# Performance work log

Measured on AMD Instinct MI355X. Metric: run time of the kernel, lower is better.

Reference implementation:

```python
import jax, jax.numpy as jnp
import numpy as np

D_MODEL = 1024
NUM_HEADS = 16
D_K = D_MODEL // NUM_HEADS
D_FF = 4096
EPS = 1e-5


def setup_inputs() -> dict:
    key = jax.random.key(0)
    ks = jax.random.split(key, 16)
    B, S = 2, 2048
    s_attn = 1.0 / np.sqrt(D_MODEL)
    s_ff1 = 1.0 / np.sqrt(D_MODEL)
    s_ff2 = 1.0 / np.sqrt(D_FF)
    return {
        "x": jax.random.normal(ks[0], (B, S, D_MODEL), jnp.float32),
        "Wq": jax.random.normal(ks[1], (D_MODEL, D_MODEL), jnp.float32) * s_attn,
        "bq": jnp.zeros((D_MODEL,), jnp.float32),
        "Wk": jax.random.normal(ks[2], (D_MODEL, D_MODEL), jnp.float32) * s_attn,
        "bk": jnp.zeros((D_MODEL,), jnp.float32),
        "Wv": jax.random.normal(ks[3], (D_MODEL, D_MODEL), jnp.float32) * s_attn,
        "bv": jnp.zeros((D_MODEL,), jnp.float32),
        "Wo": jax.random.normal(ks[4], (D_MODEL, D_MODEL), jnp.float32) * s_attn,
        "bo": jnp.zeros((D_MODEL,), jnp.float32),
        "W1": jax.random.normal(ks[5], (D_MODEL, D_FF), jnp.float32) * s_ff1,
        "b1": jnp.zeros((D_FF,), jnp.float32),
        "W2": jax.random.normal(ks[6], (D_FF, D_MODEL), jnp.float32) * s_ff2,
        "b2": jnp.zeros((D_MODEL,), jnp.float32),
        "g1": jnp.ones((D_MODEL,), jnp.float32),
        "be1": jnp.zeros((D_MODEL,), jnp.float32),
        "g2": jnp.ones((D_MODEL,), jnp.float32),
        "be2": jnp.zeros((D_MODEL,), jnp.float32),
    }


def _layernorm(x, g, b):
    m = jnp.mean(x, axis=-1, keepdims=True)
    v = jnp.mean(jnp.square(x - m), axis=-1, keepdims=True)
    return (x - m) * jax.lax.rsqrt(v + EPS) * g + b


def _split_heads(x, B, S):
    # (B, S, D) -> (B, H, S, d_k)
    return x.reshape(B, S, NUM_HEADS, D_K).transpose(0, 2, 1, 3)


def reference(x, Wq, bq, Wk, bk, Wv, bv, Wo, bo, W1, b1, W2, b2, g1, be1, g2, be2):
    B, S, _ = x.shape
    Q = _split_heads(x @ Wq + bq, B, S)
    K = _split_heads(x @ Wk + bk, B, S)
    V = _split_heads(x @ Wv + bv, B, S)
    scores = jnp.einsum("bhqd,bhkd->bhqk", Q, K) / np.sqrt(D_K).astype(np.float32)
    attn = jax.nn.softmax(scores, axis=-1)  # dropout is identity (p=0 / eval)
    ctx = jnp.einsum("bhqk,bhkd->bhqd", attn, V)
    ctx = ctx.transpose(0, 2, 1, 3).reshape(B, S, D_MODEL)
    attn_out = ctx @ Wo + bo
    h = _layernorm(x + attn_out, g1, be1)
    ff = jax.nn.relu(h @ W1 + b1) @ W2 + b2
    out = _layernorm(h + ff, g2, be2)
    return out, attn
```

## Files before the change

### kernel.cpp

```cpp
#include <hip/hip_runtime.h>
#include <cstddef>
#include <cstdint>

#define D_MODEL 1024
#define NUM_HEADS 16
#define DK 64
#define D_FF 4096
#define SEQ 2048
#define BATCH 2
#define EPS 1e-5f

typedef unsigned short u16;
typedef __attribute__((ext_vector_type(8))) short bf16x8;
typedef __attribute__((ext_vector_type(8))) unsigned short us8;
typedef __attribute__((ext_vector_type(4))) unsigned short us4;
typedef __attribute__((ext_vector_type(4))) float f32x4;

#define SBAR() asm volatile("s_barrier" ::: "memory")

__device__ __forceinline__ u16 f2b(float f) {
    unsigned u = __float_as_uint(f);
    u += 0x7fffu + ((u >> 16) & 1u);
    return (u16)(u >> 16);
}
__device__ __forceinline__ float b2f(u16 v) {
    return __uint_as_float((unsigned)v << 16);
}

__device__ __forceinline__ void gload16(const void* g, void* l) {
    __builtin_amdgcn_global_load_lds(
        (const __attribute__((address_space(1))) void*)g,
        (__attribute__((address_space(3))) void*)l, 16, 0, 0);
}

__device__ __forceinline__ void stage_half(
    const u16* __restrict__ g, int ld, long kbase, int h,
    u16* dst, int tid, int wid)
{
#pragma unroll
    for (int r = 0; r < 2; ++r) {
        const int ci  = r * 512 + tid;
        const int row = ci >> 2;
        const int wd  = ci & 3;
        const int f   = (row + (row >> 2)) & 3;
        const long src = (long)row * ld + kbase + (long)(h * 4 + (wd ^ f)) * 8;
        gload16(g + src, dst + (r * 512 + wid * 64) * 8);
    }
}

__device__ __forceinline__ bf16x8 frag64(const u16* base, int ks, int row, int g) {
    const int f = (row + (row >> 2)) & 3;
    return *(const bf16x8*)&base[ks * 8192 + row * 32 + ((g ^ f) * 8)];
}

template<int KTOT, bool RELU>
__global__ __launch_bounds__(512, 2) void gemm256(
    const u16* __restrict__ Abf, const u16* __restrict__ BT,
    const float* __restrict__ bias0, u16* __restrict__ C0,
    int ldc, int nx)
{
    constexpr int NT = KTOT / 64;
    __shared__ u16 lds[2][32768];

    const int tid = threadIdx.x;
    const int wid = tid >> 6, l = tid & 63;
    const int r16 = l & 15, g = l >> 4;
    const int wr = wid >> 2, wc = wid & 3;

    const int nwg = gridDim.x;
    const int q = nwg >> 3, rr = nwg & 7;
    const int xcd = blockIdx.x & 7, idx = blockIdx.x >> 3;
    const int wg = (xcd < rr ? xcd * (q + 1) : rr * (q + 1) + (xcd - rr) * q) + idx;
    const long bm = (long)(wg / nx) * 256;
    const long bn = (long)(wg % nx) * 256;

    const u16* Ag = Abf + bm * KTOT;
    const u16* Bg = BT + bn * KTOT;

    f32x4 acc[8][4];
#pragma unroll
    for (int i = 0; i < 8; ++i)
#pragma unroll
        for (int n = 0; n < 4; ++n)
            acc[i][n] = (f32x4){0.f, 0.f, 0.f, 0.f};

    stage_half(Ag, KTOT, 0, 0, &lds[0][0],     tid, wid);
    stage_half(Ag, KTOT, 0, 1, &lds[0][8192],  tid, wid);
    stage_half(Bg, KTOT, 0, 0, &lds[0][16384], tid, wid);
    stage_half(Bg, KTOT, 0, 1, &lds[0][24576], tid, wid);
    if (NT > 1) {
        stage_half(Ag, KTOT, 64, 0, &lds[1][0],     tid, wid);
        stage_half(Bg, KTOT, 64, 0, &lds[1][16384], tid, wid);
    }
    asm volatile("s_waitcnt vmcnt(4)" ::: "memory");
    SBAR();

    for (int t = 0; t < NT; ++t) {
        u16* cur = &lds[t & 1][0];
        u16* nxt = &lds[(t + 1) & 1][0];
        const long k1 = (long)(t + 1) * 64;
        const long k2 = (long)(t + 2) * 64;
        const bool s1 = (t + 1 < NT), s2 = (t + 2 < NT);

        bf16x8 a0[4], b0[4];
#pragma unroll
        for (int i = 0; i < 4; ++i) {
            a0[i] = frag64(cur,         0, wr * 128 + i * 16 + r16, g);
            b0[i] = frag64(cur + 16384, 0, wc * 64  + i * 16 + r16, g);
        }
        if (s1) stage_half(Ag, KTOT, k1, 1, nxt + 8192, tid, wid);
        SBAR();
        __builtin_amdgcn_s_setprio(1);
#pragma unroll
        for (int i = 0; i < 4; ++i)
#pragma unroll
            for (int n = 0; n < 4; ++n)
                acc[i][n] = __builtin_amdgcn_mfma_f32_16x16x32_bf16(
                    a0[i], b0[n], acc[i][n], 0, 0, 0);
        __builtin_amdgcn_s_setprio(0);
        SBAR();

        bf16x8 a1[4];
#pragma unroll
        for (int i = 0; i < 4; ++i)
            a1[i] = frag64(cur, 0, wr * 128 + (i + 4) * 16 + r16, g);
        if (s1) stage_half(Bg, KTOT, k1, 1, nxt + 24576, tid, wid);
        SBAR();
        __builtin_amdgcn_s_setprio(1);
#pragma unroll
        for (int i = 0; i < 4; ++i)
#pragma unroll
            for (int n = 0; n < 4; ++n)
                acc[i + 4][n] = __builtin_amdgcn_mfma_f32_16x16x32_bf16(
                    a1[i], b0[n], acc[i + 4][n], 0, 0, 0);
        __builtin_amdgcn_s_setprio(0);
        SBAR();

        bf16x8 a2[4], b1[4];
#pragma unroll
        for (int i = 0; i < 4; ++i) {
            a2[i] = frag64(cur,         1, wr * 128 + i * 16 + r16, g);
            b1[i] = frag64(cur + 16384, 1, wc * 64  + i * 16 + r16, g);
        }
        if (s2) stage_half(Ag, KTOT, k2, 0, cur, tid, wid);
        SBAR();
        __builtin_amdgcn_s_setprio(1);
#pragma unroll
        for (int i = 0; i < 4; ++i)
#pragma unroll
            for (int n = 0; n < 4; ++n)
                acc[i][n] = __builtin_amdgcn_mfma_f32_16x16x32_bf16(
                    a2[i], b1[n], acc[i][n], 0, 0, 0);
        __builtin_amdgcn_s_setprio(0);
        SBAR();

        bf16x8 a3[4];
#pragma unroll
        for (int i = 0; i < 4; ++i)
            a3[i] = frag64(cur, 1, wr * 128 + (i + 4) * 16 + r16, g);
        if (s2) stage_half(Bg, KTOT, k2, 0, cur + 16384, tid, wid);
        SBAR();
        __builtin_amdgcn_s_setprio(1);
#pragma unroll
        for (int i = 0; i < 4; ++i)
#pragma unroll
            for (int n = 0; n < 4; ++n)
                acc[i + 4][n] = __builtin_amdgcn_mfma_f32_16x16x32_bf16(
                    a3[i], b1[n], acc[i + 4][n], 0, 0, 0);
        __builtin_amdgcn_s_setprio(0);
        if (s2)      asm volatile("s_waitcnt vmcnt(4)" ::: "memory");
        else if (s1) asm volatile("s_waitcnt vmcnt(0)" ::: "memory");
        SBAR();
    }

    const long crow0 = bm + wr * 128 + g * 4;
    const long ccol0 = bn + wc * 64 + r16;
#pragma unroll
    for (int n = 0; n < 4; ++n) {
        const long col = ccol0 + n * 16;
        const float bv = bias0[col];
#pragma unroll
        for (int i = 0; i < 8; ++i)
#pragma unroll
            for (int j = 0; j < 4; ++j) {
                const long row = crow0 + i * 16 + j;
                float v = acc[i][n][j] + bv;
                if (RELU) v = fmaxf(v, 0.f);
                C0[row * (long)ldc + col] = f2b(v);
            }
    }
}

template<bool RELU, int NSPLIT>
__global__ __launch_bounds__(256) void gemm_mfma(
    const u16* __restrict__ Abf, const u16* __restrict__ BT,
    const float* __restrict__ bias0, const float* __restrict__ bias1,
    const float* __restrict__ bias2,
    u16* __restrict__ C0, u16* __restrict__ C1, u16* __restrict__ C2,
    int lda, int ldb, int ldc, int K, int nx)
{
    constexpr int BM = 128, BN = 128;
    constexpr int MI = 4, NI = 4;
    constexpr int RA = 2, RB = 2;
    constexpr int TILE = (BM + BN) * 32;

    __shared__ u16 sm[2][TILE];

    const int tid = threadIdx.x;
    const int w = tid >> 6, l = tid & 63;
    const int r16 = l & 15, g = l >> 4;
    const int wr = w >> 1, wc = w & 1;

    const int nwg = gridDim.x;
    const int q = nwg >> 3, rr = nwg & 7;
    const int xcd = blockIdx.x & 7, idx = blockIdx.x >> 3;
    const int wg = (xcd < rr ? xcd * (q + 1) : rr * (q + 1) + (xcd - rr) * q) + idx;
    const long bm = (long)(wg / nx) * BM;
    const long bn = (long)(wg % nx) * BN;

    f32x4 acc[MI][NI];
#pragma unroll
    for (int mi = 0; mi < MI; ++mi)
#pragma unroll
        for (int ni = 0; ni < NI; ++ni)
            acc[mi][ni] = (f32x4){0.f, 0.f, 0.f, 0.f};

    long aOff[RA], bOff[RB];
#pragma unroll
    for (int r = 0; r < RA; ++r) {
        int c = r * 256 + tid;
        aOff[r] = (long)(bm + (c >> 2)) * lda + (c & 3) * 8;
    }
#pragma unroll
    for (int r = 0; r < RB; ++r) {
        int c = r * 256 + tid;
        bOff[r] = (long)(bn + (c >> 2)) * ldb + (c & 3) * 8;
    }

#pragma unroll
    for (int r = 0; r < RA; ++r)
        gload16(Abf + aOff[r], &sm[0][0] + (r * 256 + w * 64) * 8);
#pragma unroll
    for (int r = 0; r < RB; ++r)
        gload16(BT + bOff[r], &sm[0][BM * 32] + (r * 256 + w * 64) * 8);
    __syncthreads();

    int cur = 0;
    for (int k0 = 0; k0 < K; k0 += 32) {
        if (k0 + 32 < K) {
            const int nxt = cur ^ 1;
#pragma unroll
            for (int r = 0; r < RA; ++r)
                gload16(Abf + aOff[r] + k0 + 32, &sm[nxt][0] + (r * 256 + w * 64) * 8);
#pragma unroll
            for (int r = 0; r < RB; ++r)
                gload16(BT + bOff[r] + k0 + 32, &sm[nxt][BM * 32] + (r * 256 + w * 64) * 8);
        }

        const u16* smA = &sm[cur][0];
        const u16* smB = &sm[cur][BM * 32];
        bf16x8 af[MI], bfr[NI];
#pragma unroll
        for (int mi = 0; mi < MI; ++mi)
            af[mi] = *(const bf16x8*)&smA[(wr * 64 + mi * 16 + r16) * 32 + g * 8];
#pragma unroll
        for (int ni = 0; ni < NI; ++ni)
            bfr[ni] = *(const bf16x8*)&smB[(wc * 64 + ni * 16 + r16) * 32 + g * 8];
#pragma unroll
        for (int mi = 0; mi < MI; ++mi)
#pragma unroll
            for (int ni = 0; ni < NI; ++ni)
                acc[mi][ni] = __builtin_amdgcn_mfma_f32_16x16x32_bf16(
                    af[mi], bfr[ni], acc[mi][ni], 0, 0, 0);

        __syncthreads();
        cur ^= 1;
    }

    const long crow0 = bm + wr * 64 + g * 4;

    if (NSPLIT == 3 && bn >= 2048) {
        const int btok = (int)(crow0 >> 11);
        const int kr0  = (int)(crow0 & 2047);
        const long ccolV = bn + wc * 64 + r16 - 2048;
#pragma unroll
        for (int ni = 0; ni < NI; ++ni) {
            const long col = ccolV + ni * 16;
            const int h = (int)(col >> 6), d = (int)(col & 63);
            const float bv = bias2[col];
            const long vrow = ((long)(btok * 16 + h) * 64 + d) * (long)SEQ;
#pragma unroll
            for (int mi = 0; mi < MI; ++mi) {
                us4 pv;
#pragma unroll
                for (int j = 0; j < 4; ++j)
                    pv[j] = f2b(acc[mi][ni][j] + bv);
                *(us4*)&C2[vrow + kr0 + mi * 16] = pv;
            }
        }
        return;
    }

    u16* Cb = C0; const float* bp = bias0; long coff = 0;
    if (NSPLIT == 3) {
        const int grp = (int)(bn >> 10);
        if (grp == 1) { Cb = C1; bp = bias1; }
        coff = (long)grp << 10;
    }
    const long ccol0 = bn + wc * 64 + r16 - coff;
#pragma unroll
    for (int ni = 0; ni < NI; ++ni) {
        const long col = ccol0 + ni * 16;
        const float bv = bp[col];
#pragma unroll
        for (int mi = 0; mi < MI; ++mi) {
#pragma unroll
            for (int j = 0; j < 4; ++j) {
                const long row = crow0 + mi * 16 + j;
                float v = acc[mi][ni][j] + bv;
                if (RELU) v = fmaxf(v, 0.f);
                Cb[row * (long)ldc + col] = f2b(v);
            }
        }
    }
}

#define QBLK 128
#define KBLK 64
#define NTT (SEQ / KBLK)
#define C2E 0.18033688f

__global__ __launch_bounds__(256) void flash_attn(
    const u16* __restrict__ Qg, const u16* __restrict__ Kg,
    const u16* __restrict__ Vt, float* __restrict__ attn,
    u16* __restrict__ ctx)
{
    __shared__ u16 smem[16384];
    __shared__ u16 Ps[4][2048];

    u16* const Qs  = smem;
    u16* const kb0 = smem + 8192;
    u16* const kb1 = smem;

    const int tid = threadIdx.x;
    const int w = tid >> 6, l = tid & 63;
    const int r16 = l & 15, g = l >> 4;

    const int wg = (blockIdx.x & 7) * (gridDim.x >> 3) + (blockIdx.x >> 3);
    const int qb = wg & 15, z = wg >> 4;
    const int b = z >> 4, h = z & 15;
    const long q0 = (long)qb * QBLK;

    const long kBase = ((long)b * SEQ) * D_MODEL + h * DK;
    const long vBase = (long)z * DK * SEQ;

#pragma unroll
    for (int r = 0; r < 4; ++r) {
        int c = r * 256 + tid;
        int row = c >> 3, bl = c & 7;
        long src = ((long)b * SEQ + q0 + row) * D_MODEL + h * DK
                 + ((bl ^ (row & 7)) * 8);
        gload16(Qg + src, Qs + (r * 256 + w * 64) * 8);
    }
#pragma unroll
    for (int r = 0; r < 2; ++r) {
        int c = r * 256 + tid;
        int row = c >> 3, bl = c & 7;
        gload16(Kg + kBase + (long)row * D_MODEL + ((bl ^ (row & 7)) * 8),
                kb0 + (r * 256 + w * 64) * 8);
    }
    __syncthreads();

    bf16x8 qf[2][2];
#pragma unroll
    for (int qi = 0; qi < 2; ++qi)
#pragma unroll
        for (int ks = 0; ks < 2; ++ks)
            qf[qi][ks] = *(const bf16x8*)
                &Qs[(w * 32 + qi * 16 + r16) * 64 + (((ks * 4 + g) ^ (r16 & 7)) * 8)];
    __syncthreads();

    float lrun[2] = {0.f, 0.f};

    for (int t = 0; t < NTT; ++t) {
        if (t + 1 < NTT) {
            u16* kdst = ((t + 1) & 1) ? kb1 : kb0;
            const long kro = (long)(t + 1) * KBLK;
#pragma unroll
            for (int r = 0; r < 2; ++r) {
                int c = r * 256 + tid;
                int row = c >> 3, bl = c & 7;
                gload16(Kg + kBase + (kro + row) * D_MODEL + ((bl ^ (row & 7)) * 8),
                        kdst + (r * 256 + w * 64) * 8);
            }
        }
        const u16* kcur = (t & 1) ? kb1 : kb0;

        f32x4 sT[4][2];
#pragma unroll
        for (int ki = 0; ki < 4; ++ki)
#pragma unroll
            for (int qi = 0; qi < 2; ++qi) sT[ki][qi] = (f32x4){0.f, 0.f, 0.f, 0.f};

        __builtin_amdgcn_s_setprio(1);
#pragma unroll
        for (int ks = 0; ks < 2; ++ks) {
            bf16x8 kf[4];
#pragma unroll
            for (int ki = 0; ki < 4; ++ki)
                kf[ki] = *(const bf16x8*)
                    &kcur[(ki * 16 + r16) * 64 + (((ks * 4 + g) ^ (r16 & 7)) * 8)];
#pragma unroll
            for (int ki = 0; ki < 4; ++ki)
#pragma unroll
                for (int qi = 0; qi < 2; ++qi)
                    sT[ki][qi] = __builtin_amdgcn_mfma_f32_16x16x32_bf16(
                        kf[ki], qf[qi][ks], sT[ki][qi], 0, 0, 0);
        }
        __builtin_amdgcn_s_setprio(0);

#pragma unroll
        for (int qi = 0; qi < 2; ++qi) {
            float ls = 0.f;
#pragma unroll
            for (int ki = 0; ki < 4; ++ki)
#pragma unroll
                for (int j = 0; j < 4; ++j)
                    ls += exp2f(sT[ki][qi][j] * C2E);
            ls += __shfl_xor(ls, 16);
            ls += __shfl_xor(ls, 32);
            lrun[qi] += ls;
        }
        __syncthreads();
    }

    const float il[2] = {1.0f / lrun[0], 1.0f / lrun[1]};

    u16* const p2b0 = smem + 8192;
    u16* const p2b1 = smem;
#pragma unroll
    for (int r = 0; r < 2; ++r) {
        int c = r * 256 + tid;
        int row = c >> 3, bl = c & 7;
        gload16(Kg + kBase + (long)row * D_MODEL + ((bl ^ (row & 7)) * 8),
                p2b0 + (r * 256 + w * 64) * 8);
        gload16(Vt + vBase + (long)row * SEQ + ((bl ^ (row & 7)) * 8),
                p2b0 + 4096 + (r * 256 + w * 64) * 8);
    }
    __syncthreads();

    f32x4 acc2[2][4];
#pragma unroll
    for (int mi = 0; mi < 2; ++mi)
#pragma unroll
        for (int ni = 0; ni < 4; ++ni) acc2[mi][ni] = (f32x4){0.f, 0.f, 0.f, 0.f};

    const long arow0 = ((long)z * SEQ + q0 + w * 32) * (long)SEQ;

    for (int t = 0; t < NTT; ++t) {
        const int k0 = t * KBLK;
        if (t + 1 < NTT) {
            u16* dst = ((t + 1) & 1) ? p2b1 : p2b0;
            const long kro = (long)(t + 1) * KBLK;
#pragma unroll
            for (int r = 0; r < 2; ++r) {
                int c = r * 256 + tid;
                int row = c >> 3, bl = c & 7;
                gload16(Kg + kBase + (kro + row) * D_MODEL + ((bl ^ (row & 7)) * 8),
                        dst + (r * 256 + w * 64) * 8);
                gload16(Vt + vBase + (long)row * SEQ + kro + ((bl ^ (row & 7)) * 8),
                        dst + 4096 + (r * 256 + w * 64) * 8);
            }
        }
        const u16* kcur = (t & 1) ? p2b1 : p2b0;
        const u16* vcur = kcur + 4096;

        f32x4 sT[4][2];
#pragma unroll
        for (int ki = 0; ki < 4; ++ki)
#pragma unroll
            for (int qi = 0; qi < 2; ++qi) sT[ki][qi] = (f32x4){0.f, 0.f, 0.f, 0.f};

        __builtin_amdgcn_s_setprio(1);
#pragma unroll
        for (int ks = 0; ks < 2; ++ks) {
            bf16x8 kf[4];
#pragma unroll
            for (int ki = 0; ki < 4; ++ki)
                kf[ki] = *(const bf16x8*)
                    &kcur[(ki * 16 + r16) * 64 + (((ks * 4 + g) ^ (r16 & 7)) * 8)];
#pragma unroll
            for (int ki = 0; ki < 4; ++ki)
#pragma unroll
                for (int qi = 0; qi < 2; ++qi)
                    sT[ki][qi] = __builtin_amdgcn_mfma_f32_16x16x32_bf16(
                        kf[ki], qf[qi][ks], sT[ki][qi], 0, 0, 0);
        }
        __builtin_amdgcn_s_setprio(0);

#pragma unroll
        for (int qi = 0; qi < 2; ++qi) {
            const long ar = arow0 + (long)(qi * 16 + r16) * SEQ + k0 + g * 4;
            const int prow = (qi * 16 + r16) * 64;
#pragma unroll
            for (int ki = 0; ki < 4; ++ki) {
                f32x4 p;
                p[0] = exp2f(sT[ki][qi][0] * C2E) * il[qi];
                p[1] = exp2f(sT[ki][qi][1] * C2E) * il[qi];
                p[2] = exp2f(sT[ki][qi][2] * C2E) * il[qi];
                p[3] = exp2f(sT[ki][qi][3] * C2E) * il[qi];
                __builtin_nontemporal_store(p, (f32x4*)&attn[ar + ki * 16]);
                us4 pb;
                pb[0] = f2b(p[0]); pb[1] = f2b(p[1]);
                pb[2] = f2b(p[2]); pb[3] = f2b(p[3]);
                const int kblk = 2 * ki + (g >> 1);
                *(us4*)&Ps[w][prow + ((kblk ^ (r16 & 7)) << 3) + ((g & 1) << 2)] = pb;
            }
        }

        __builtin_amdgcn_s_setprio(1);
#pragma unroll
        for (int ks = 0; ks < 2; ++ks) {
            bf16x8 pf[2], vf[4];
#pragma unroll
            for (int mi = 0; mi < 2; ++mi)
                pf[mi] = *(const bf16x8*)
                    &Ps[w][(mi * 16 + r16) * 64 + (((ks * 4 + g) ^ (r16 & 7)) << 3)];
#pragma unroll
            for (int ni = 0; ni < 4; ++ni)
                vf[ni] = *(const bf16x8*)
                    &vcur[(ni * 16 + r16) * 64 + (((ks * 4 + g) ^ (r16 & 7)) * 8)];
#pragma unroll
            for (int mi = 0; mi < 2; ++mi)
#pragma unroll
                for (int ni = 0; ni < 4; ++ni)
                    acc2[mi][ni] = __builtin_amdgcn_mfma_f32_16x16x32_bf16(
                        pf[mi], vf[ni], acc2[mi][ni], 0, 0, 0);
        }
        __builtin_amdgcn_s_setprio(0);
        __syncthreads();
    }

#pragma unroll
    for (int mi = 0; mi < 2; ++mi)
#pragma unroll
        for (int j = 0; j < 4; ++j) {
            const long grow = (long)b * SEQ + q0 + w * 32 + mi * 16 + g * 4 + j;
#pragma unroll
            for (int ni = 0; ni < 4; ++ni)
                ctx[grow * D_MODEL + h * DK + ni * 16 + r16] = f2b(acc2[mi][ni][j]);
        }
}

__device__ __forceinline__ void tr32(
    const float* __restrict__ W, u16* __restrict__ Wt, int R, int C,
    int bx, int by, int tx, int ty, float (*t)[33])
{
    const long c = (long)bx * 32 + tx;
    const long r0 = (long)by * 32;
#pragma unroll
    for (int j = 0; j < 32; j += 8)
        t[ty + j][tx] = W[(r0 + ty + j) * C + c];
    __syncthreads();
    const long r = r0 + tx;
#pragma unroll
    for (int j = 0; j < 32; j += 8)
        Wt[((long)bx * 32 + ty + j) * R + r] = f2b(t[tx][ty + j]);
}

__global__ __launch_bounds__(256) void preproc(
    const float* __restrict__ x, u16* __restrict__ x_bf,
    const float* __restrict__ Wq, const float* __restrict__ Wk,
    const float* __restrict__ Wv, const float* __restrict__ Wo,
    u16* __restrict__ Wqkvo_t,
    const float* __restrict__ W1, u16* __restrict__ W1t,
    const float* __restrict__ W2, u16* __restrict__ W2t)
{
    __shared__ float t[32][33];
    int bid = blockIdx.x;
    const int tx = threadIdx.x & 31, ty = threadIdx.x >> 5;

    if (bid < 2048) {
        long i = ((long)bid * 256 + threadIdx.x) * 8;
        float4 a = *(const float4*)(x + i);
        float4 b = *(const float4*)(x + i + 4);
        us8 o;
        o[0] = f2b(a.x); o[1] = f2b(a.y); o[2] = f2b(a.z); o[3] = f2b(a.w);
        o[4] = f2b(b.x); o[5] = f2b(b.y); o[6] = f2b(b.z); o[7] = f2b(b.w);
        *(us8*)(x_bf + i) = o;
        return;
    }
    bid -= 2048;
    if (bid < 4096) {
        const int z = bid >> 10, rem = bid & 1023;
        const float* W = (z == 0) ? Wq : (z == 1) ? Wk : (z == 2) ? Wv : Wo;
        tr32(W, Wqkvo_t + (size_t)z * D_MODEL * D_MODEL, D_MODEL, D_MODEL,
             rem & 31, rem >> 5, tx, ty, t);
        return;
    }
    bid -= 4096;
    if (bid < 4096) {
        tr32(W1, W1t, D_MODEL, D_FF, bid & 127, bid >> 7, tx, ty, t);
        return;
    }
    bid -= 4096;
    {
        tr32(W2, W2t, D_FF, D_MODEL, bid & 31, bid >> 5, tx, ty, t);
    }
}

template<int OM>
__global__ __launch_bounds__(256) void add_ln_kernel(
    const u16* __restrict__ a, const u16* __restrict__ b,
    const float* __restrict__ g, const float* __restrict__ be,
    void* __restrict__ outp)
{
    const int l = threadIdx.x & 63, w = threadIdx.x >> 6;
    const long row = (long)blockIdx.x * 4 + w;
    const long base = row * D_MODEL;

    float xv[16];
#pragma unroll
    for (int c = 0; c < 2; ++c) {
        const long off = c * 512 + l * 8;
        us8 av = *(const us8*)(a + base + off);
        us8 bv = *(const us8*)(b + base + off);
#pragma unroll
        for (int i = 0; i < 8; ++i)
            xv[c * 8 + i] = b2f(av[i]) + b2f(bv[i]);
    }

    float s = 0.f;
#pragma unroll
    for (int i = 0; i < 16; ++i) s += xv[i];
#pragma unroll
    for (int off = 1; off < 64; off <<= 1) s += __shfl_xor(s, off);
    const float mean = s * (1.0f / D_MODEL);

    float ss = 0.f;
#pragma unroll
    for (int i = 0; i < 16; ++i) {
        xv[i] -= mean;
        ss += xv[i] * xv[i];
    }
#pragma unroll
    for (int off = 1; off < 64; off <<= 1) ss += __shfl_xor(ss, off);
    const float rs = rsqrtf(ss * (1.0f / D_MODEL) + EPS);

#pragma unroll
    for (int c = 0; c < 2; ++c) {
        const long off = c * 512 + l * 8;
        float4 g0 = *(const float4*)(g + off);
        float4 g1 = *(const float4*)(g + off + 4);
        float4 b0 = *(const float4*)(be + off);
        float4 b1 = *(const float4*)(be + off + 4);
        float o[8];
        o[0] = xv[c*8+0] * rs * g0.x + b0.x;
        o[1] = xv[c*8+1] * rs * g0.y + b0.y;
        o[2] = xv[c*8+2] * rs * g0.z + b0.z;
        o[3] = xv[c*8+3] * rs * g0.w + b0.w;
        o[4] = xv[c*8+4] * rs * g1.x + b1.x;
        o[5] = xv[c*8+5] * rs * g1.y + b1.y;
        o[6] = xv[c*8+6] * rs * g1.z + b1.z;
        o[7] = xv[c*8+7] * rs * g1.w + b1.w;
        if (OM == 0) {
            float4 v0 = {o[0], o[1], o[2], o[3]};
            float4 v1 = {o[4], o[5], o[6], o[7]};
            *(float4*)((float*)outp + base + off) = v0;
            *(float4*)((float*)outp + base + off + 4) = v1;
        } else {
            us8 ob;
#pragma unroll
            for (int i = 0; i < 8; ++i) ob[i] = f2b(o[i]);
            *(us8*)((u16*)outp + base + off) = ob;
        }
    }
}

extern "C" void kernel_launch(void* const* d_in, const int* in_sizes, int n_in,
                              void* d_out, int out_size, void* d_ws, size_t ws_size,
                              hipStream_t stream)
{
    const float* x   = (const float*)d_in[0];
    const float* Wq  = (const float*)d_in[1];
    const float* bq  = (const float*)d_in[2];
    const float* Wk  = (const float*)d_in[3];
    const float* bk  = (const float*)d_in[4];
    const float* Wv  = (const float*)d_in[5];
    const float* bv  = (const float*)d_in[6];
    const float* Wo  = (const float*)d_in[7];
    const float* bo  = (const float*)d_in[8];
    const float* W1  = (const float*)d_in[9];
    const float* b1  = (const float*)d_in[10];
    const float* W2  = (const float*)d_in[11];
    const float* b2  = (const float*)d_in[12];
    const float* g1  = (const float*)d_in[13];
    const float* be1 = (const float*)d_in[14];
    const float* g2  = (const float*)d_in[15];
    const float* be2 = (const float*)d_in[16];

    float* out  = (float*)d_out;
    float* attn = out + (size_t)BATCH * SEQ * D_MODEL;

    char* ws = (char*)d_ws;
    const size_t MB = 1u << 20;
    u16* x_bf    = (u16*)(ws);
    u16* Q_bf    = (u16*)(ws + 8 * MB);
    u16* K_bf    = (u16*)(ws + 16 * MB);
    u16* Vt      = (u16*)(ws + 24 * MB);
    u16* spare   = (u16*)(ws + 32 * MB);
    u16* Wqkvo_t = (u16*)(ws + 40 * MB);
    u16* W1t     = (u16*)(ws + 48 * MB);
    u16* W2t     = (u16*)(ws + 56 * MB);
    u16* ff1_bf  = (u16*)(ws + 64 * MB);
    u16* ctx_bf  = (u16*)(ws + 96 * MB);
    u16* Wot     = Wqkvo_t + (size_t)3 * D_MODEL * D_MODEL;
    u16* h_bf    = K_bf;
    u16* ao_bf   = spare;
    u16* ff2_bf  = Vt;

    const int M = BATCH * SEQ;
    dim3 T(256);

    preproc<<<dim3(2048 + 3 * 4096), T, 0, stream>>>(
        x, x_bf, Wq, Wk, Wv, Wo, Wqkvo_t, W1, W1t, W2, W2t);

    gemm_mfma<false, 3><<<dim3((M / 128) * 24), T, 0, stream>>>(
        x_bf, Wqkvo_t, bq, bk, bv, Q_bf, K_bf, Vt,
        D_MODEL, D_MODEL, D_MODEL, D_MODEL, 24);

    flash_attn<<<dim3((SEQ / QBLK) * BATCH * NUM_HEADS), T, 0, stream>>>(
        Q_bf, K_bf, Vt, attn, ctx_bf);

    gemm_mfma<false, 1><<<dim3((M / 128) * 8), T, 0, stream>>>(
        ctx_bf, Wot, bo, nullptr, nullptr, ao_bf, nullptr, nullptr,
        D_MODEL, D_MODEL, D_MODEL, D_MODEL, 8);

    add_ln_kernel<1><<<dim3(M / 4), T, 0, stream>>>(x_bf, ao_bf, g1, be1, h_bf);

    gemm256<D_MODEL, true><<<dim3((M / 256) * (D_FF / 256)), dim3(512), 0, stream>>>(
        h_bf, W1t, b1, ff1_bf, D_FF, D_FF / 256);

    gemm_mfma<false, 1><<<dim3((M / 128) * 8), T, 0, stream>>>(
        ff1_bf, W2t, b2, nullptr, nullptr, ff2_bf, nullptr, nullptr,
        D_FF, D_FF, D_MODEL, D_FF, 8);

    add_ln_kernel<0><<<dim3(M / 4), T, 0, stream>>>(h_bf, ff2_bf, g2, be2, out);
}
```

Before: 424.8 us.

## Add 128x64 GEMM for N=1024 projections and split V transpose into separate kernel

Adds a new gemm_n64 kernel with 128x64 tiles and uses it for the Wo and W2 projections. This doubles the number of workgroups on the N=1024 GEMMs (512 instead of 256) to fill more compute units, at the cost of more A-tile reloads. The fused transposed V store in the QKV GEMM epilogue is replaced by a plain row-major store plus a separate shared-memory transpose kernel. That removes the strided scatter writes but adds an extra launch and an extra pass over V.

```diff
diff --git a/kernel.cpp b/kernel.cpp
--- a/kernel.cpp
+++ b/kernel.cpp
@@ -277,36 +277,14 @@
         cur ^= 1;
     }
 
-    const long crow0 = bm + wr * 64 + g * 4;
-
-    if (NSPLIT == 3 && bn >= 2048) {
-        const int btok = (int)(crow0 >> 11);
-        const int kr0  = (int)(crow0 & 2047);
-        const long ccolV = bn + wc * 64 + r16 - 2048;
-#pragma unroll
-        for (int ni = 0; ni < NI; ++ni) {
-            const long col = ccolV + ni * 16;
-            const int h = (int)(col >> 6), d = (int)(col & 63);
-            const float bv = bias2[col];
-            const long vrow = ((long)(btok * 16 + h) * 64 + d) * (long)SEQ;
-#pragma unroll
-            for (int mi = 0; mi < MI; ++mi) {
-                us4 pv;
-#pragma unroll
-                for (int j = 0; j < 4; ++j)
-                    pv[j] = f2b(acc[mi][ni][j] + bv);
-                *(us4*)&C2[vrow + kr0 + mi * 16] = pv;
-            }
-        }
-        return;
-    }
-
     u16* Cb = C0; const float* bp = bias0; long coff = 0;
     if (NSPLIT == 3) {
         const int grp = (int)(bn >> 10);
-        if (grp == 1) { Cb = C1; bp = bias1; }
+        if (grp == 1)      { Cb = C1; bp = bias1; }
+        else if (grp == 2) { Cb = C2; bp = bias2; }
         coff = (long)grp << 10;
     }
+    const long crow0 = bm + wr * 64 + g * 4;
     const long ccol0 = bn + wc * 64 + r16 - coff;
 #pragma unroll
     for (int ni = 0; ni < NI; ++ni) {
@@ -320,6 +298,108 @@
                 float v = acc[mi][ni][j] + bv;
                 if (RELU) v = fmaxf(v, 0.f);
                 Cb[row * (long)ldc + col] = f2b(v);
+            }
+        }
+    }
+}
+
+template<bool RELU>
+__global__ __launch_bounds__(256) void gemm_n64(
+    const u16* __restrict__ Abf, const u16* __restrict__ BT,
+    const float* __restrict__ bias, u16* __restrict__ C,
+    int lda, int ldb, int ldc, int K, int nx)
+{
+    constexpr int BM = 128, BN = 64;
+    constexpr int MI = 2, NI = 4;
+    constexpr int RA = 2, RB = 1;
+    constexpr int TILE = (BM + BN) * 32;
+
+    __shared__ u16 sm[2][TILE];
+
+    const int tid = threadIdx.x;
+    const int w = tid >> 6, l = tid & 63;
+    const int r16 = l & 15, g = l >> 4;
+
+    const int nwg = gridDim.x;
+    const int q = nwg >> 3, rr = nwg & 7;
+    const int xcd = blockIdx.x & 7, idx = blockIdx.x >> 3;
+    const int wg = (xcd < rr ? xcd * (q + 1) : rr * (q + 1) + (xcd - rr) * q) + idx;
+    const long bm = (long)(wg / nx) * BM;
+    const long bn = (long)(wg % nx) * BN;
+
+    f32x4 acc[MI][NI];
+#pragma unroll
+    for (int mi = 0; mi < MI; ++mi)
+#pragma unroll
+        for (int ni = 0; ni < NI; ++ni)
+            acc[mi][ni] = (f32x4){0.f, 0.f, 0.f, 0.f};
+
+    long aOff[RA], bOff[RB];
+#pragma unroll
+    for (int r = 0; r < RA; ++r) {
+        int c = r * 256 + tid;
+        aOff[r] = (long)(bm + (c >> 2)) * lda + (c & 3) * 8;
+    }
+#pragma unroll
+    for (int r = 0; r < RB; ++r) {
+        int c = r * 256 + tid;
+        bOff[r] = (long)(bn + (c >> 2)) * ldb + (c & 3) * 8;
+    }
+
+#pragma unroll
+    for (int r = 0; r < RA; ++r)
+        gload16(Abf + aOff[r], &sm[0][0] + (r * 256 + w * 64) * 8);
+#pragma unroll
+    for (int r = 0; r < RB; ++r)
+        gload16(BT + bOff[r], &sm[0][BM * 32] + (r * 256 + w * 64) * 8);
+    __syncthreads();
+
+    int cur = 0;
+    for (int k0 = 0; k0 < K; k0 += 32) {
+        if (k0 + 32 < K) {
+            const int nxt = cur ^ 1;
+#pragma unroll
+            for (int r = 0; r < RA; ++r)
+                gload16(Abf + aOff[r] + k0 + 32, &sm[nxt][0] + (r * 256 + w * 64) * 8);
+#pragma unroll
+            for (int r = 0; r < RB; ++r)
+                gload16(BT + bOff[r] + k0 + 32, &sm[nxt][BM * 32] + (r * 256 + w * 64) * 8);
+        }
+
+        const u16* smA = &sm[cur][0];
+        const u16* smB = &sm[cur][BM * 32];
+        bf16x8 af[MI], bfr[NI];
+#pragma unroll
+        for (int mi = 0; mi < MI; ++mi)
+            af[mi] = *(const bf16x8*)&smA[(w * 32 + mi * 16 + r16) * 32 + g * 8];
+#pragma unroll
+        for (int ni = 0; ni < NI; ++ni)
+            bfr[ni] = *(const bf16x8*)&smB[(ni * 16 + r16) * 32 + g * 8];
+#pragma unroll
+        for (int mi = 0; mi < MI; ++mi)
+#pragma unroll
+            for (int ni = 0; ni < NI; ++ni)
+                acc[mi][ni] = __builtin_amdgcn_mfma_f32_16x16x32_bf16(
+                    af[mi], bfr[ni], acc[mi][ni], 0, 0, 0);
+
+        __syncthreads();
+        cur ^= 1;
+    }
+
+    const long crow0 = bm + w * 32 + g * 4;
+    const long ccol0 = bn + r16;
+#pragma unroll
+    for (int ni = 0; ni < NI; ++ni) {
+        const long col = ccol0 + ni * 16;
+        const float bv = bias[col];
+#pragma unroll
+        for (int mi = 0; mi < MI; ++mi) {
+#pragma unroll
+            for (int j = 0; j < 4; ++j) {
+                const long row = crow0 + mi * 16 + j;
+                float v = acc[mi][ni][j] + bv;
+                if (RELU) v = fmaxf(v, 0.f);
+                C[row * (long)ldc + col] = f2b(v);
             }
         }
     }
@@ -607,6 +687,23 @@
     {
         tr32(W2, W2t, D_FF, D_MODEL, bid & 31, bid >> 5, tx, ty, t);
     }
+}
+
+__global__ __launch_bounds__(256) void transpose_v(
+    const u16* __restrict__ V, u16* __restrict__ Vt)
+{
+    __shared__ u16 t[32][33];
+    const int z = blockIdx.z, b = z >> 4, h = z & 15;
+    const int tx = threadIdx.x & 31, ty = threadIdx.x >> 5;
+    const long k0 = (long)blockIdx.x * 32;
+    const long d0 = (long)blockIdx.y * 32;
+#pragma unroll
+    for (int j = 0; j < 32; j += 8)
+        t[ty + j][tx] = V[((long)b * SEQ + k0 + ty + j) * D_MODEL + h * DK + d0 + tx];
+    __syncthreads();
+#pragma unroll
+    for (int j = 0; j < 32; j += 8)
+        Vt[((long)z * DK + d0 + ty + j) * SEQ + k0 + tx] = t[tx][ty + j];
 }
 
 template<int OM>
@@ -708,7 +805,7 @@
     u16* Q_bf    = (u16*)(ws + 8 * MB);
     u16* K_bf    = (u16*)(ws + 16 * MB);
     u16* Vt      = (u16*)(ws + 24 * MB);
-    u16* spare   = (u16*)(ws + 32 * MB);
+    u16* V_bf    = (u16*)(ws + 32 * MB);
     u16* Wqkvo_t = (u16*)(ws + 40 * MB);
     u16* W1t     = (u16*)(ws + 48 * MB);
     u16* W2t     = (u16*)(ws + 56 * MB);
@@ -716,7 +813,7 @@
     u16* ctx_bf  = (u16*)(ws + 96 * MB);
     u16* Wot     = Wqkvo_t + (size_t)3 * D_MODEL * D_MODEL;
     u16* h_bf    = K_bf;
-    u16* ao_bf   = spare;
+    u16* ao_bf   = V_bf;
     u16* ff2_bf  = Vt;
 
     const int M = BATCH * SEQ;
@@ -726,24 +823,24 @@
         x, x_bf, Wq, Wk, Wv, Wo, Wqkvo_t, W1, W1t, W2, W2t);
 
     gemm_mfma<false, 3><<<dim3((M / 128) * 24), T, 0, stream>>>(
-        x_bf, Wqkvo_t, bq, bk, bv, Q_bf, K_bf, Vt,
+        x_bf, Wqkvo_t, bq, bk, bv, Q_bf, K_bf, V_bf,
         D_MODEL, D_MODEL, D_MODEL, D_MODEL, 24);
+
+    transpose_v<<<dim3(SEQ / 32, DK / 32, BATCH * NUM_HEADS), T, 0, stream>>>(V_bf, Vt);
 
     flash_attn<<<dim3((SEQ / QBLK) * BATCH * NUM_HEADS), T, 0, stream>>>(
         Q_bf, K_bf, Vt, attn, ctx_bf);
 
-    gemm_mfma<false, 1><<<dim3((M / 128) * 8), T, 0, stream>>>(
-        ctx_bf, Wot, bo, nullptr, nullptr, ao_bf, nullptr, nullptr,
-        D_MODEL, D_MODEL, D_MODEL, D_MODEL, 8);
+    gemm_n64<false><<<dim3((M / 128) * 16), T, 0, stream>>>(
+        ctx_bf, Wot, bo, ao_bf, D_MODEL, D_MODEL, D_MODEL, D_MODEL, 16);
 
     add_ln_kernel<1><<<dim3(M / 4), T, 0, stream>>>(x_bf, ao_bf, g1, be1, h_bf);
 
     gemm256<D_MODEL, true><<<dim3((M / 256) * (D_FF / 256)), dim3(512), 0, stream>>>(
         h_bf, W1t, b1, ff1_bf, D_FF, D_FF / 256);
 
-    gemm_mfma<false, 1><<<dim3((M / 128) * 8), T, 0, stream>>>(
-        ff1_bf, W2t, b2, nullptr, nullptr, ff2_bf, nullptr, nullptr,
-        D_FF, D_FF, D_MODEL, D_FF, 8);
+    gemm_n64<false><<<dim3((M / 128) * 16), T, 0, stream>>>(
+        ff1_bf, W2t, b2, ff2_bf, D_FF, D_FF, D_MODEL, D_FF, 16);
 
     add_ln_kernel<0><<<dim3(M / 4), T, 0, stream>>>(h_bf, ff2_bf, g2, be2, out);
 }
```

After: 409.7 us. -3.6%, faster.
